# Kernel optimization log

Hardware: AMD Instinct MI355X
Metric: run time of the kernel (lower is better)

## Reference

```python
import jax, jax.numpy as jnp
import numpy as np

N = 50000      # nodes
E = 800000     # edges (avg degree 16)
F_IN = 512
HID = 128
OUT = 64
NIDX = 1000


def setup_inputs() -> dict:
    key = jax.random.key(0)
    ks = jax.random.split(key, 7)
    x = jax.random.normal(ks[0], (N, F_IN), dtype=jnp.float32)
    edge_src = jax.random.randint(ks[1], (E,), 0, N)
    edge_dst = jax.random.randint(ks[2], (E,), 0, N)
    edge_weight = jax.random.uniform(ks[3], (E,), dtype=jnp.float32)
    W0 = jax.random.normal(ks[4], (F_IN, HID), dtype=jnp.float32) * (1.0 / np.sqrt(F_IN))
    W1 = jax.random.normal(ks[5], (HID, OUT), dtype=jnp.float32) * (1.0 / np.sqrt(HID))
    idx = jax.random.randint(ks[6], (NIDX,), 0, N)
    return {"x": x, "W0": W0, "W1": W1, "edge_weight": edge_weight,
            "edge_src": edge_src, "edge_dst": edge_dst, "idx": idx}


def _spmm(edge_src, edge_dst, edge_weight, h):
    # sparse adj @ h in COO form: gather rows by src, weight, scatter-add to dst
    msg = h[edge_src] * edge_weight[:, None]          # [E, d]
    return jax.ops.segment_sum(msg, edge_dst, num_segments=N)  # [N, d]


def reference(x, W0, W1, edge_weight, edge_src, edge_dst, idx):
    # layer 0: GraphConvolution (x @ W then adj spmm), relu; dropout omitted (eval)
    h = jax.nn.relu(_spmm(edge_src, edge_dst, edge_weight, x @ W0))  # [N, HID]
    # layer 1: final GraphConvolution, no activation
    out = _spmm(edge_src, edge_dst, edge_weight, h @ W1)             # [N, OUT]
    return out[idx]                                                  # [NIDX, OUT]
```

## Files before the change

kernel.cpp:

```cpp
#include <hip/hip_runtime.h>
#include <hip/hip_bf16.h>

#define N_NODES 50000
#define F_IN    512
#define HID     128
#define OUT_F   64
#define NIDX    1000
#define E_NUM   800000
#define CAP     48
#define NSC1    256
#define NGB     782
#define NSCAN2  768

typedef __attribute__((ext_vector_type(8))) short short8;
typedef __attribute__((ext_vector_type(4))) float f32x4;

__device__ inline ushort f2bf(float f) {
    __hip_bfloat16 h = __float2bfloat16(f);
    return *reinterpret_cast<ushort*>(&h);
}
__device__ inline float bf2f(ushort u) {
    return __uint_as_float(((uint)u) << 16);
}
__device__ inline short8 pack8(f32x4 a, f32x4 b) {
    short8 r;
    r[0] = (short)f2bf(a[0]); r[1] = (short)f2bf(a[1]);
    r[2] = (short)f2bf(a[2]); r[3] = (short)f2bf(a[3]);
    r[4] = (short)f2bf(b[0]); r[5] = (short)f2bf(b[1]);
    r[6] = (short)f2bf(b[2]); r[7] = (short)f2bf(b[3]);
    return r;
}

#define GLOAD_LDS16(g, l) __builtin_amdgcn_global_load_lds( \
    (const __attribute__((address_space(1))) unsigned int*)(g), \
    (__attribute__((address_space(3))) unsigned int*)(l), 16, 0, 0)

__global__ __launch_bounds__(256) void prep_kernel(const float* __restrict__ W0,
                                                   ushort* __restrict__ W0t,
                                                   const int* __restrict__ idx,
                                                   ushort* __restrict__ jmap) {
    const int b = blockIdx.x;
    if (b < 64) {
        __shared__ float tl[32][33];
        const int k0 = (b & 15) * 32, n0 = (b >> 4) * 32;
        const int tx = threadIdx.x & 31, ty = threadIdx.x >> 5;
#pragma unroll
        for (int i = 0; i < 4; ++i)
            tl[ty + i * 8][tx] = W0[(size_t)(k0 + ty + i * 8) * HID + n0 + tx];
        __syncthreads();
#pragma unroll
        for (int i = 0; i < 4; ++i) {
            const int n = ty + i * 8;
            W0t[(size_t)(n0 + n) * F_IN + k0 + tx] = f2bf(tl[tx][n]);
        }
    } else {
        const int j = (b - 64) * 256 + threadIdx.x;
        if (j < NIDX) jmap[idx[j]] = (ushort)(j + 1);
    }
}

__global__ __launch_bounds__(256, 5) void fused_gemm_scan1(
        const float* __restrict__ x, const ushort* __restrict__ W0t,
        ushort* __restrict__ XW0b,
        const int* __restrict__ esrc, const int* __restrict__ edst,
        const float* __restrict__ ew, const ushort* __restrict__ jmap,
        int* __restrict__ countsA, int2* __restrict__ bktA,
        ushort* __restrict__ flags) {
    __shared__ __align__(16) char smem[32768];

    if (blockIdx.x < NSC1) {
        for (int q = blockIdx.x * 256 + threadIdx.x; q < E_NUM / 4; q += NSC1 * 256) {
            const int e0 = q * 4;
            const int4   d4 = *(const int4*)(edst + e0);
            const int4   s4 = *(const int4*)(esrc + e0);
            const float4 w4 = *(const float4*)(ew + e0);
#define DOIT(DD, SS, WW) { const int rep = jmap[DD]; if (rep) { \
        const int r = rep - 1; const int c = atomicAdd(&countsA[r], 1); \
        if (c < CAP) bktA[(size_t)r * CAP + c] = make_int2(SS, __float_as_int(WW)); \
        flags[SS] = 1; } }
            DOIT(d4.x, s4.x, w4.x) DOIT(d4.y, s4.y, w4.y)
            DOIT(d4.z, s4.z, w4.z) DOIT(d4.w, s4.w, w4.w)
#undef DOIT
        }
        return;
    }

    const int t = threadIdx.x;
    const int w = t >> 6, lane = t & 63;
    const int wr = w >> 1, wc = w & 1;
    const int lr = lane & 15, lk = lane >> 4;
    const int m0 = (blockIdx.x - NSC1) * 64;

    char* lA = smem;
    char* lB = smem + 16384;
    f32x4 acc[2][4] = {};

    for (int kt = 0; kt < 8; ++kt) {
        const int k0 = kt * 64;
#pragma unroll
        for (int i = 0; i < 4; ++i) {
            const int o = i * 256 + t;
            {
                const int row = o >> 4, c = o & 15;
                int ga = m0 + row; if (ga > N_NODES - 1) ga = N_NODES - 1;
                const float* g = x + (size_t)ga * F_IN + k0 + ((c ^ ((row & 7) << 1)) << 2);
                GLOAD_LDS16(g, lA + (i * 256 + w * 64) * 16);
            }
            {
                const int row = o >> 3, c = o & 7;
                const ushort* g = W0t + (size_t)row * F_IN + k0 + ((c ^ (row & 7)) << 3);
                GLOAD_LDS16(g, lB + (i * 256 + w * 64) * 16);
            }
        }
        __syncthreads();

#pragma unroll
        for (int kk = 0; kk < 2; ++kk) {
            short8 a[2], b[4];
#pragma unroll
            for (int mi = 0; mi < 2; ++mi) {
                const int R = wr * 32 + mi * 16 + lr;
                const int cs = (kk * 8 + lk * 2) ^ ((R & 7) << 1);
                const f32x4 lo = *(const f32x4*)(lA + R * 256 + (cs << 4));
                const f32x4 hi = *(const f32x4*)(lA + R * 256 + (cs << 4) + 16);
                a[mi] = pack8(lo, hi);
            }
#pragma unroll
            for (int ni = 0; ni < 4; ++ni) {
                const int Rb = wc * 64 + ni * 16 + lr;
                const int cs = (kk * 4 + lk) ^ (Rb & 7);
                b[ni] = *(const short8*)(lB + Rb * 128 + (cs << 4));
            }
#pragma unroll
            for (int mi = 0; mi < 2; ++mi)
#pragma unroll
                for (int ni = 0; ni < 4; ++ni)
                    acc[mi][ni] = __builtin_amdgcn_mfma_f32_16x16x32_bf16(
                        a[mi], b[ni], acc[mi][ni], 0, 0, 0);
        }
        __syncthreads();
    }

    float* ep = (float*)smem + w * (16 * 68);
#pragma unroll
    for (int mi = 0; mi < 2; ++mi) {
        __syncthreads();
#pragma unroll
        for (int ni = 0; ni < 4; ++ni)
#pragma unroll
            for (int r = 0; r < 4; ++r)
                ep[(lk * 4 + r) * 68 + ni * 16 + lr] = acc[mi][ni][r];
        __syncthreads();
        const int rr = lane >> 2, cq = lane & 3;
        const int grow = m0 + wr * 32 + mi * 16 + rr;
        alignas(16) float vv[16];
#pragma unroll
        for (int j = 0; j < 4; ++j)
            *(f32x4*)&vv[j * 4] = *(const f32x4*)&ep[rr * 68 + cq * 16 + j * 4];
        if (grow < N_NODES) {
            alignas(16) ushort us[16];
#pragma unroll
            for (int jj = 0; jj < 16; ++jj) us[jj] = f2bf(vv[jj]);
            ushort* orow = XW0b + (size_t)grow * HID + wc * 64 + cq * 16;
            *(uint4*)(orow)     = *(const uint4*)&us[0];
            *(uint4*)(orow + 8) = *(const uint4*)&us[8];
        }
    }
}

__global__ __launch_bounds__(256) void scan2_kernel(const int* __restrict__ esrc,
                                                    const int* __restrict__ edst,
                                                    const float* __restrict__ ew,
                                                    const ushort* __restrict__ flags,
                                                    int* __restrict__ countsB,
                                                    int2* __restrict__ bktB) {
    for (int q = blockIdx.x * 256 + threadIdx.x; q < E_NUM / 4; q += NSCAN2 * 256) {
        const int e0 = q * 4;
        const int4   d4 = *(const int4*)(edst + e0);
        const int4   s4 = *(const int4*)(esrc + e0);
        const float4 w4 = *(const float4*)(ew + e0);
#define DO2(DD, SS, WW) { if (flags[DD]) { \
        const int c = atomicAdd(&countsB[DD], 1); \
        if (c < CAP) bktB[(size_t)(DD) * CAP + c] = make_int2(SS, __float_as_int(WW)); } }
        DO2(d4.x, s4.x, w4.x) DO2(d4.y, s4.y, w4.y)
        DO2(d4.z, s4.z, w4.z) DO2(d4.w, s4.w, w4.w)
#undef DO2
    }
}

__global__ __launch_bounds__(256) void spmm1_kernel(const ushort* __restrict__ XW0b,
                                                    const ushort* __restrict__ flags,
                                                    const int* __restrict__ countsB,
                                                    const int2* __restrict__ bktB,
                                                    ushort* __restrict__ H) {
    const int wv = threadIdx.x >> 6, lane = threadIdx.x & 63;
    const int g = lane >> 4, s = lane & 15;
    for (int n = blockIdx.x * 4 + wv; n < N_NODES; n += gridDim.x * 4) {
        if (!flags[n]) continue;
        const int deg = min(countsB[n], CAP);
        const int2* brow = bktB + (size_t)n * CAP;
        float acc[8] = {};
        for (int c = 0; c < deg; c += 4) {
            const int e = c + g;
            if (e < deg) {
                const int2 p = brow[e];
                const float wt = __int_as_float(p.y);
                const uint4 v = *(const uint4*)(XW0b + (size_t)p.x * HID + s * 8);
                acc[0] += wt * bf2f((ushort)(v.x & 0xffffu));
                acc[1] += wt * bf2f((ushort)(v.x >> 16));
                acc[2] += wt * bf2f((ushort)(v.y & 0xffffu));
                acc[3] += wt * bf2f((ushort)(v.y >> 16));
                acc[4] += wt * bf2f((ushort)(v.z & 0xffffu));
                acc[5] += wt * bf2f((ushort)(v.z >> 16));
                acc[6] += wt * bf2f((ushort)(v.w & 0xffffu));
                acc[7] += wt * bf2f((ushort)(v.w >> 16));
            }
        }
#pragma unroll
        for (int j = 0; j < 8; ++j) {
            acc[j] += __shfl_xor(acc[j], 16);
            acc[j] += __shfl_xor(acc[j], 32);
        }
        if (g == 0) {
            uint4 o;
            o.x = (uint)f2bf(fmaxf(acc[0], 0.f)) | ((uint)f2bf(fmaxf(acc[1], 0.f)) << 16);
            o.y = (uint)f2bf(fmaxf(acc[2], 0.f)) | ((uint)f2bf(fmaxf(acc[3], 0.f)) << 16);
            o.z = (uint)f2bf(fmaxf(acc[4], 0.f)) | ((uint)f2bf(fmaxf(acc[5], 0.f)) << 16);
            o.w = (uint)f2bf(fmaxf(acc[6], 0.f)) | ((uint)f2bf(fmaxf(acc[7], 0.f)) << 16);
            *(uint4*)(H + (size_t)n * HID + s * 8) = o;
        }
    }
}

__global__ __launch_bounds__(64) void spmm2_kernel(const ushort* __restrict__ H,
                                                   const float* __restrict__ W1,
                                                   const int* __restrict__ idx,
                                                   const ushort* __restrict__ jmap,
                                                   const int* __restrict__ countsA,
                                                   const int2* __restrict__ bktA,
                                                   float* __restrict__ outp) {
    __shared__ float aggs[HID];
    const int j = blockIdx.x, lane = threadIdx.x;
    const int r = (int)jmap[idx[j]] - 1;
    const int deg = min(countsA[r], CAP);
    float a0 = 0.f, a1 = 0.f;
    for (int c = 0; c < deg; ++c) {
        const int2 p = bktA[(size_t)r * CAP + c];
        const float wt = __int_as_float(p.y);
        const uint v = *(const uint*)(H + (size_t)p.x * HID + 2 * lane);
        a0 += wt * bf2f((ushort)(v & 0xffffu));
        a1 += wt * bf2f((ushort)(v >> 16));
    }
    aggs[2 * lane] = a0; aggs[2 * lane + 1] = a1;
    __syncthreads();
    float s = 0.f;
#pragma unroll 8
    for (int k = 0; k < HID; ++k) s += aggs[k] * W1[k * OUT_F + lane];
    outp[(size_t)j * OUT_F + lane] = s;
}

extern "C" void kernel_launch(void* const* d_in, const int* in_sizes, int n_in,
                              void* d_out, int out_size, void* d_ws, size_t ws_size,
                              hipStream_t stream) {
    const float* x    = (const float*)d_in[0];
    const float* W0   = (const float*)d_in[1];
    const float* W1   = (const float*)d_in[2];
    const float* ew   = (const float*)d_in[3];
    const int*   esrc = (const int*)d_in[4];
    const int*   edst = (const int*)d_in[5];
    const int*   idx  = (const int*)d_in[6];
    float* outp = (float*)d_out;

    char* ws = (char*)d_ws;
    ushort* XW0b   = (ushort*)(ws);
    ushort* H      = (ushort*)(ws + 12800000);
    ushort* W0t    = (ushort*)(ws + 25600000);
    int2*   bktA   = (int2*)  (ws + 25731072);
    int2*   bktB   = (int2*)  (ws + 26115072);
    char*   zbase  = ws + 45315072;
    int*    countsA = (int*)   (zbase);
    int*    countsB = (int*)   (zbase + 4096);
    ushort* flags   = (ushort*)(zbase + 208896);
    ushort* jmap    = (ushort*)(zbase + 309248);
    hipMemsetAsync(zbase, 0, 409600, stream);

    prep_kernel     <<<68, 256, 0, stream>>>(W0, W0t, idx, jmap);
    fused_gemm_scan1<<<NSC1 + NGB, 256, 0, stream>>>(
                        x, W0t, XW0b, esrc, edst, ew, jmap, countsA, bktA, flags);
    scan2_kernel    <<<NSCAN2, 256, 0, stream>>>(esrc, edst, ew, flags, countsB, bktB);
    spmm1_kernel    <<<2048, 256, 0, stream>>>(XW0b, flags, countsB, bktB, H);
    spmm2_kernel    <<<NIDX, 64, 0, stream>>>(H, W1, idx, jmap, countsA, bktA, outp);
}
```

Baseline: 88.80 us.

## Split fused GEMM+scan1 kernel into separate scan1 and GEMM kernels

Separates the first edge scan from the dense X@W0 GEMM into its own kernel with 768 blocks, and launches the GEMM as a standalone kernel after scan2. This undoes the horizontal fusion that overlapped the scan with the GEMM. It may relieve contention between atomic-heavy scan blocks and GEMM blocks, but adds a kernel launch and drops the overlap.

After: 95.76 us. 7.8% more time.

```diff
diff --git a/kernel.cpp b/kernel.cpp
--- a/kernel.cpp
+++ b/kernel.cpp
@@ -8,9 +8,8 @@
 #define NIDX    1000
 #define E_NUM   800000
 #define CAP     48
-#define NSC1    256
 #define NGB     782
-#define NSCAN2  768
+#define NSCAN   768
 
 typedef __attribute__((ext_vector_type(8))) short short8;
 typedef __attribute__((ext_vector_type(4))) float f32x4;
@@ -59,112 +58,25 @@
     }
 }
 
-__global__ __launch_bounds__(256, 5) void fused_gemm_scan1(
-        const float* __restrict__ x, const ushort* __restrict__ W0t,
-        ushort* __restrict__ XW0b,
-        const int* __restrict__ esrc, const int* __restrict__ edst,
-        const float* __restrict__ ew, const ushort* __restrict__ jmap,
-        int* __restrict__ countsA, int2* __restrict__ bktA,
-        ushort* __restrict__ flags) {
-    __shared__ __align__(16) char smem[32768];
-
-    if (blockIdx.x < NSC1) {
-        for (int q = blockIdx.x * 256 + threadIdx.x; q < E_NUM / 4; q += NSC1 * 256) {
-            const int e0 = q * 4;
-            const int4   d4 = *(const int4*)(edst + e0);
-            const int4   s4 = *(const int4*)(esrc + e0);
-            const float4 w4 = *(const float4*)(ew + e0);
+__global__ __launch_bounds__(256) void scan1_kernel(const int* __restrict__ esrc,
+                                                    const int* __restrict__ edst,
+                                                    const float* __restrict__ ew,
+                                                    const ushort* __restrict__ jmap,
+                                                    int* __restrict__ countsA,
+                                                    int2* __restrict__ bktA,
+                                                    ushort* __restrict__ flags) {
+    for (int q = blockIdx.x * 256 + threadIdx.x; q < E_NUM / 4; q += NSCAN * 256) {
+        const int e0 = q * 4;
+        const int4   d4 = *(const int4*)(edst + e0);
+        const int4   s4 = *(const int4*)(esrc + e0);
+        const float4 w4 = *(const float4*)(ew + e0);
 #define DOIT(DD, SS, WW) { const int rep = jmap[DD]; if (rep) { \
         const int r = rep - 1; const int c = atomicAdd(&countsA[r], 1); \
         if (c < CAP) bktA[(size_t)r * CAP + c] = make_int2(SS, __float_as_int(WW)); \
         flags[SS] = 1; } }
-            DOIT(d4.x, s4.x, w4.x) DOIT(d4.y, s4.y, w4.y)
-            DOIT(d4.z, s4.z, w4.z) DOIT(d4.w, s4.w, w4.w)
+        DOIT(d4.x, s4.x, w4.x) DOIT(d4.y, s4.y, w4.y)
+        DOIT(d4.z, s4.z, w4.z) DOIT(d4.w, s4.w, w4.w)
 #undef DOIT
-        }
-        return;
-    }
-
-    const int t = threadIdx.x;
-    const int w = t >> 6, lane = t & 63;
-    const int wr = w >> 1, wc = w & 1;
-    const int lr = lane & 15, lk = lane >> 4;
-    const int m0 = (blockIdx.x - NSC1) * 64;
-
-    char* lA = smem;
-    char* lB = smem + 16384;
-    f32x4 acc[2][4] = {};
-
-    for (int kt = 0; kt < 8; ++kt) {
-        const int k0 = kt * 64;
-#pragma unroll
-        for (int i = 0; i < 4; ++i) {
-            const int o = i * 256 + t;
-            {
-                const int row = o >> 4, c = o & 15;
-                int ga = m0 + row; if (ga > N_NODES - 1) ga = N_NODES - 1;
-                const float* g = x + (size_t)ga * F_IN + k0 + ((c ^ ((row & 7) << 1)) << 2);
-                GLOAD_LDS16(g, lA + (i * 256 + w * 64) * 16);
-            }
-            {
-                const int row = o >> 3, c = o & 7;
-                const ushort* g = W0t + (size_t)row * F_IN + k0 + ((c ^ (row & 7)) << 3);
-                GLOAD_LDS16(g, lB + (i * 256 + w * 64) * 16);
-            }
-        }
-        __syncthreads();
-
-#pragma unroll
-        for (int kk = 0; kk < 2; ++kk) {
-            short8 a[2], b[4];
-#pragma unroll
-            for (int mi = 0; mi < 2; ++mi) {
-                const int R = wr * 32 + mi * 16 + lr;
-                const int cs = (kk * 8 + lk * 2) ^ ((R & 7) << 1);
-                const f32x4 lo = *(const f32x4*)(lA + R * 256 + (cs << 4));
-                const f32x4 hi = *(const f32x4*)(lA + R * 256 + (cs << 4) + 16);
-                a[mi] = pack8(lo, hi);
-            }
-#pragma unroll
-            for (int ni = 0; ni < 4; ++ni) {
-                const int Rb = wc * 64 + ni * 16 + lr;
-                const int cs = (kk * 4 + lk) ^ (Rb & 7);
-                b[ni] = *(const short8*)(lB + Rb * 128 + (cs << 4));
-            }
-#pragma unroll
-            for (int mi = 0; mi < 2; ++mi)
-#pragma unroll
-                for (int ni = 0; ni < 4; ++ni)
-                    acc[mi][ni] = __builtin_amdgcn_mfma_f32_16x16x32_bf16(
-                        a[mi], b[ni], acc[mi][ni], 0, 0, 0);
-        }
-        __syncthreads();
-    }
-
-    float* ep = (float*)smem + w * (16 * 68);
-#pragma unroll
-    for (int mi = 0; mi < 2; ++mi) {
-        __syncthreads();
-#pragma unroll
-        for (int ni = 0; ni < 4; ++ni)
-#pragma unroll
-            for (int r = 0; r < 4; ++r)
-                ep[(lk * 4 + r) * 68 + ni * 16 + lr] = acc[mi][ni][r];
-        __syncthreads();
-        const int rr = lane >> 2, cq = lane & 3;
-        const int grow = m0 + wr * 32 + mi * 16 + rr;
-        alignas(16) float vv[16];
-#pragma unroll
-        for (int j = 0; j < 4; ++j)
-            *(f32x4*)&vv[j * 4] = *(const f32x4*)&ep[rr * 68 + cq * 16 + j * 4];
-        if (grow < N_NODES) {
-            alignas(16) ushort us[16];
-#pragma unroll
-            for (int jj = 0; jj < 16; ++jj) us[jj] = f2bf(vv[jj]);
-            ushort* orow = XW0b + (size_t)grow * HID + wc * 64 + cq * 16;
-            *(uint4*)(orow)     = *(const uint4*)&us[0];
-            *(uint4*)(orow + 8) = *(const uint4*)&us[8];
-        }
     }
 }
 
@@ -174,7 +86,7 @@
                                                     const ushort* __restrict__ flags,
                                                     int* __restrict__ countsB,
                                                     int2* __restrict__ bktB) {
-    for (int q = blockIdx.x * 256 + threadIdx.x; q < E_NUM / 4; q += NSCAN2 * 256) {
+    for (int q = blockIdx.x * 256 + threadIdx.x; q < E_NUM / 4; q += NSCAN * 256) {
         const int e0 = q * 4;
         const int4   d4 = *(const int4*)(edst + e0);
         const int4   s4 = *(const int4*)(esrc + e0);
@@ -185,6 +97,94 @@
         DO2(d4.x, s4.x, w4.x) DO2(d4.y, s4.y, w4.y)
         DO2(d4.z, s4.z, w4.z) DO2(d4.w, s4.w, w4.w)
 #undef DO2
+    }
+}
+
+__global__ __launch_bounds__(256, 5) void gemm1_kernel(const float* __restrict__ x,
+                                                       const ushort* __restrict__ W0t,
+                                                       ushort* __restrict__ XW0b) {
+    __shared__ __align__(16) char smem[32768];
+
+    const int t = threadIdx.x;
+    const int w = t >> 6, lane = t & 63;
+    const int wr = w >> 1, wc = w & 1;
+    const int lr = lane & 15, lk = lane >> 4;
+    const int m0 = blockIdx.x * 64;
+
+    char* lA = smem;
+    char* lB = smem + 16384;
+    f32x4 acc[2][4] = {};
+
+    for (int kt = 0; kt < 8; ++kt) {
+        const int k0 = kt * 64;
+#pragma unroll
+        for (int i = 0; i < 4; ++i) {
+            const int o = i * 256 + t;
+            {
+                const int row = o >> 4, c = o & 15;
+                int ga = m0 + row; if (ga > N_NODES - 1) ga = N_NODES - 1;
+                const float* g = x + (size_t)ga * F_IN + k0 + ((c ^ ((row & 7) << 1)) << 2);
+                GLOAD_LDS16(g, lA + (i * 256 + w * 64) * 16);
+            }
+            {
+                const int row = o >> 3, c = o & 7;
+                const ushort* g = W0t + (size_t)row * F_IN + k0 + ((c ^ (row & 7)) << 3);
+                GLOAD_LDS16(g, lB + (i * 256 + w * 64) * 16);
+            }
+        }
+        __syncthreads();
+
+#pragma unroll
+        for (int kk = 0; kk < 2; ++kk) {
+            short8 a[2], b[4];
+#pragma unroll
+            for (int mi = 0; mi < 2; ++mi) {
+                const int R = wr * 32 + mi * 16 + lr;
+                const int cs = (kk * 8 + lk * 2) ^ ((R & 7) << 1);
+                const f32x4 lo = *(const f32x4*)(lA + R * 256 + (cs << 4));
+                const f32x4 hi = *(const f32x4*)(lA + R * 256 + (cs << 4) + 16);
+                a[mi] = pack8(lo, hi);
+            }
+#pragma unroll
+            for (int ni = 0; ni < 4; ++ni) {
+                const int Rb = wc * 64 + ni * 16 + lr;
+                const int cs = (kk * 4 + lk) ^ (Rb & 7);
+                b[ni] = *(const short8*)(lB + Rb * 128 + (cs << 4));
+            }
+#pragma unroll
+            for (int mi = 0; mi < 2; ++mi)
+#pragma unroll
+                for (int ni = 0; ni < 4; ++ni)
+                    acc[mi][ni] = __builtin_amdgcn_mfma_f32_16x16x32_bf16(
+                        a[mi], b[ni], acc[mi][ni], 0, 0, 0);
+        }
+        __syncthreads();
+    }
+
+    float* ep = (float*)smem + w * (16 * 68);
+#pragma unroll
+    for (int mi = 0; mi < 2; ++mi) {
+        __syncthreads();
+#pragma unroll
+        for (int ni = 0; ni < 4; ++ni)
+#pragma unroll
+            for (int r = 0; r < 4; ++r)
+                ep[(lk * 4 + r) * 68 + ni * 16 + lr] = acc[mi][ni][r];
+        __syncthreads();
+        const int rr = lane >> 2, cq = lane & 3;
+        const int grow = m0 + wr * 32 + mi * 16 + rr;
+        alignas(16) float vv[16];
+#pragma unroll
+        for (int j = 0; j < 4; ++j)
+            *(f32x4*)&vv[j * 4] = *(const f32x4*)&ep[rr * 68 + cq * 16 + j * 4];
+        if (grow < N_NODES) {
+            alignas(16) ushort us[16];
+#pragma unroll
+            for (int jj = 0; jj < 16; ++jj) us[jj] = f2bf(vv[jj]);
+            ushort* orow = XW0b + (size_t)grow * HID + wc * 64 + cq * 16;
+            *(uint4*)(orow)     = *(const uint4*)&us[0];
+            *(uint4*)(orow + 8) = *(const uint4*)&us[8];
+        }
     }
 }
 
@@ -284,10 +284,10 @@
     ushort* jmap    = (ushort*)(zbase + 309248);
     hipMemsetAsync(zbase, 0, 409600, stream);
 
-    prep_kernel     <<<68, 256, 0, stream>>>(W0, W0t, idx, jmap);
-    fused_gemm_scan1<<<NSC1 + NGB, 256, 0, stream>>>(
-                        x, W0t, XW0b, esrc, edst, ew, jmap, countsA, bktA, flags);
-    scan2_kernel    <<<NSCAN2, 256, 0, stream>>>(esrc, edst, ew, flags, countsB, bktB);
-    spmm1_kernel    <<<2048, 256, 0, stream>>>(XW0b, flags, countsB, bktB, H);
-    spmm2_kernel    <<<NIDX, 64, 0, stream>>>(H, W1, idx, jmap, countsA, bktA, outp);
-}
+    prep_kernel <<<68, 256, 0, stream>>>(W0, W0t, idx, jmap);
+    scan1_kernel<<<NSCAN, 256, 0, stream>>>(esrc, edst, ew, jmap, countsA, bktA, flags);
+    scan2_kernel<<<NSCAN, 256, 0, stream>>>(esrc, edst, ew, flags, countsB, bktB);
+    gemm1_kernel<<<NGB, 256, 0, stream>>>(x, W0t, XW0b);
+    spmm1_kernel<<<2048, 256, 0, stream>>>(XW0b, flags, countsB, bktB, H);
+    spmm2_kernel<<<NIDX, 64, 0, stream>>>(H, W1, idx, jmap, countsA, bktA, outp);
+}
```
